# Optimization experiments

Measured on AMD Instinct MI355X. Metric: run time of the kernel, lower is better.

## Reference

```python
import jax, jax.numpy as jnp
import numpy as np

B, L, ENC_D, DEC_D, ATTN_D = 64, 1024, 512, 512, 512


def setup_inputs() -> dict:
    key = jax.random.key(0)
    ks = jax.random.split(key, 8)
    s_enc = 1.0 / np.sqrt(ENC_D)
    s_dec = 1.0 / np.sqrt(DEC_D)
    s_att = 1.0 / np.sqrt(ATTN_D)
    return {
        "enc_out": jax.random.normal(ks[0], (B, L, ENC_D), dtype=jnp.float32),
        "dec_hidden": jax.random.normal(ks[1], (B, DEC_D), dtype=jnp.float32),
        # nn.Linear params (uniform(-1/sqrt(fan_in), 1/sqrt(fan_in)))
        "W_enc": jax.random.uniform(ks[2], (ENC_D, ATTN_D), jnp.float32, -s_enc, s_enc),
        "b_enc": jax.random.uniform(ks[3], (ATTN_D,), jnp.float32, -s_enc, s_enc),
        "W_dec": jax.random.uniform(ks[4], (DEC_D, ATTN_D), jnp.float32, -s_dec, s_dec),
        "b_dec": jax.random.uniform(ks[5], (ATTN_D,), jnp.float32, -s_dec, s_dec),
        "W_full": jax.random.uniform(ks[6], (ATTN_D,), jnp.float32, -s_att, s_att),
        "b_full": jax.random.uniform(ks[7], (), jnp.float32, -s_att, s_att),
    }


def reference(enc_out, dec_hidden, W_enc, b_enc, W_dec, b_dec, W_full, b_full):
    # attn1: [B, L, A]; attn2: [B, A]
    attn1 = jnp.einsum("ble,ea->bla", enc_out, W_enc) + b_enc
    attn2 = dec_hidden @ W_dec + b_dec
    # full_attn(relu(attn1 + attn2[:, None])) -> [B, L]
    attn = jnp.einsum("bla,a->bl", jax.nn.relu(attn1 + attn2[:, None, :]), W_full) + b_full
    alpha = jax.nn.softmax(attn, axis=1)  # over L
    attn_weighted_enc = jnp.einsum("ble,bl->be", enc_out, alpha)
    return attn_weighted_enc, alpha
```

## Files before the change

### kernel.cpp

```cpp
#include <hip/hip_runtime.h>
#include <hip/hip_bf16.h>

typedef __bf16 bf16x8 __attribute__((ext_vector_type(8)));
typedef float f32x16 __attribute__((ext_vector_type(16)));
typedef unsigned int u32;
typedef unsigned short u16;

#define WS_WT     0
#define WS_BIAS   524288
#define WS_LOGITS 655360

__device__ __forceinline__ u16 f2bf(float f) {
    __bf16 h = (__bf16)f;
    return __builtin_bit_cast(u16, h);
}

__device__ __forceinline__ void gload_lds16(const void* g, void* l) {
    __builtin_amdgcn_global_load_lds(
        (const __attribute__((address_space(1))) u32*)g,
        (__attribute__((address_space(3))) u32*)l, 16, 0, 0);
}

__device__ __forceinline__ bf16x8 cvt8(float4 a, float4 b) {
    bf16x8 r;
    r[0] = (__bf16)a.x; r[1] = (__bf16)a.y; r[2] = (__bf16)a.z; r[3] = (__bf16)a.w;
    r[4] = (__bf16)b.x; r[5] = (__bf16)b.y; r[6] = (__bf16)b.z; r[7] = (__bf16)b.w;
    return r;
}

__global__ void k_wt(const float* __restrict__ W, u16* __restrict__ WtP) {
    int u = blockIdx.x * 256 + threadIdx.x;
    int l = u & 63, ks = (u >> 6) & 31, p = u >> 11;
    int n = p * 32 + (l & 31);
    int k0 = ks * 16 + (l >> 5) * 8;
    u16 o[8];
    #pragma unroll
    for (int e = 0; e < 8; ++e)
        o[e] = f2bf(W[(k0 + e) * 512 + n]);
    *(uint4*)(WtP + (size_t)u * 8) = *(const uint4*)o;
}

__global__ void k_bias2(const float* __restrict__ dec, const float* __restrict__ Wd,
                        const float* __restrict__ b_dec, const float* __restrict__ b_enc,
                        float* __restrict__ bias2p, float* __restrict__ out0) {
    int blk = blockIdx.x;
    int b = blk >> 2, nc = blk & 3;
    int t = threadIdx.x;
    if (blk < 64) {
        out0[blk * 512 + t * 2] = 0.f;
        out0[blk * 512 + t * 2 + 1] = 0.f;
    }
    __shared__ float sdec[512];
    __shared__ float red[256];
    for (int k = t; k < 512; k += 256) sdec[k] = dec[b * 512 + k];
    __syncthreads();
    int n = nc * 128 + (t & 127);
    int kh = t >> 7;
    float acc = 0.f;
    int k0 = kh * 256;
    #pragma unroll 4
    for (int k = k0; k < k0 + 256; ++k)
        acc += sdec[k] * Wd[k * 512 + n];
    red[t] = acc;
    __syncthreads();
    if (t < 128) {
        int nn = nc * 128 + t;
        bias2p[b * 512 + nn] = red[t] + red[t + 128] + b_dec[nn] + b_enc[nn];
    }
}

__global__ __launch_bounds__(256, 2) void k_logits(
        const float* __restrict__ enc, const u16* __restrict__ WtP,
        const float* __restrict__ bias2p, const float* __restrict__ Wf,
        float* __restrict__ logits) {
    __shared__ __align__(16) char ldsA[32768];
    __shared__ __align__(16) char ldsB0[16384];
    __shared__ __align__(16) char ldsB1[16384];

    int t = threadIdx.x;
    int lane = t & 63;
    int w = t >> 6;
    int blk = blockIdx.x;
    int b = blk >> 3;
    int cl = lane & 31;
    int hi = lane >> 5;

    #define STAGEB(buf, p_, h_)                                                   \
        {                                                                         \
            const char* s_ = (const char*)WtP + (size_t)(p_) * 32768              \
                             + (h_) * 16384 + t * 16;                             \
            _Pragma("unroll")                                                     \
            for (int j = 0; j < 4; ++j)                                           \
                gload_lds16(s_ + j * 4096, (char*)(buf) + t * 16 + j * 4096);     \
        }
    #define STAGEA(s_)                                                            \
        {                                                                         \
            size_t base_ = ((size_t)blk * 128 + (s_) * 16) * 2048;                \
            _Pragma("unroll")                                                     \
            for (int j = 0; j < 8; ++j) {                                         \
                int u_ = t + j * 256;                                             \
                int r_ = u_ >> 7, c_ = u_ & 127;                                  \
                const char* src_ = (const char*)enc + base_ + (size_t)r_ * 2048   \
                                   + ((size_t)(c_ ^ (r_ & 7)) * 16);              \
                gload_lds16(src_, ldsA + (size_t)u_ * 16);                        \
            }                                                                     \
        }

    STAGEB(ldsB0, 0, 0)
    STAGEA(0)

    bf16x8 A[32];
    int rloc = lane & 15;
    int myswz = rloc & 7;
    int parity = (lane >> 4) & 1;
    for (int s = 0; s < 8; ++s) {
        __syncthreads();
        if ((s >> 1) == w && (s & 1) == parity) {
            #pragma unroll
            for (int f = 0; f < 32; ++f) {
                int c0 = (f * 4 + hi * 2) ^ myswz;
                int c1 = (f * 4 + hi * 2 + 1) ^ myswz;
                float4 lo = *(const float4*)(ldsA + rloc * 2048 + c0 * 16);
                float4 h4 = *(const float4*)(ldsA + rloc * 2048 + c1 * 16);
                A[f] = cvt8(lo, h4);
            }
        }
        __syncthreads();
        if (s < 7) STAGEA(s + 1)
    }
    #pragma unroll
    for (int f = 0; f < 32; ++f)
        asm volatile("" : "+v"(A[f]));

    float pr[16];
    #pragma unroll
    for (int r = 0; r < 16; ++r) pr[r] = 0.f;

    for (int p = 0; p < 16; ++p) {
        __syncthreads();
        STAGEB(ldsB1, p, 1)
        f32x16 acc0 = {};
        #pragma unroll
        for (int i = 0; i < 16; ++i) {
            uint4 braw = *(const uint4*)(ldsB0 + i * 1024 + lane * 16);
            acc0 = __builtin_amdgcn_mfma_f32_32x32x16_bf16(
                A[i], __builtin_bit_cast(bf16x8, braw), acc0, 0, 0, 0);
        }
        __syncthreads();
        if (p < 15) STAGEB(ldsB0, p + 1, 0)
        f32x16 acc1 = {};
        #pragma unroll
        for (int i = 0; i < 16; ++i) {
            uint4 braw = *(const uint4*)(ldsB1 + i * 1024 + lane * 16);
            acc1 = __builtin_amdgcn_mfma_f32_32x32x16_bf16(
                A[16 + i], __builtin_bit_cast(bf16x8, braw), acc1, 0, 0, 0);
        }
        int col = p * 32 + cl;
        float bias = bias2p[b * 512 + col];
        float wfv = Wf[col];
        #pragma unroll
        for (int r = 0; r < 16; ++r) {
            float v = acc0[r] + acc1[r] + bias;
            v = v > 0.f ? v : 0.f;
            pr[r] += v * wfv;
        }
    }

    #pragma unroll
    for (int r = 0; r < 16; ++r) {
        float v = pr[r];
        v += __shfl_xor(v, 1, 64);
        v += __shfl_xor(v, 2, 64);
        v += __shfl_xor(v, 4, 64);
        v += __shfl_xor(v, 8, 64);
        v += __shfl_xor(v, 16, 64);
        if (cl == 0)
            logits[blk * 128 + w * 32 + (r & 3) + 8 * (r >> 2) + 4 * hi] = v;
    }
}

__global__ void k_softmax(const float* __restrict__ logits, float* __restrict__ alpha) {
    int b = blockIdx.x;
    int t = threadIdx.x;
    __shared__ float red[256];
    float4 v = ((const float4*)(logits + b * 1024))[t];
    float mx = fmaxf(fmaxf(v.x, v.y), fmaxf(v.z, v.w));
    red[t] = mx;
    __syncthreads();
    for (int s = 128; s > 0; s >>= 1) {
        if (t < s) red[t] = fmaxf(red[t], red[t + s]);
        __syncthreads();
    }
    mx = red[0];
    __syncthreads();
    float4 e;
    e.x = expf(v.x - mx); e.y = expf(v.y - mx);
    e.z = expf(v.z - mx); e.w = expf(v.w - mx);
    red[t] = e.x + e.y + e.z + e.w;
    __syncthreads();
    for (int s = 128; s > 0; s >>= 1) {
        if (t < s) red[t] += red[t + s];
        __syncthreads();
    }
    float inv = 1.0f / red[0];
    float4 o;
    o.x = e.x * inv; o.y = e.y * inv; o.z = e.z * inv; o.w = e.w * inv;
    ((float4*)(alpha + b * 1024))[t] = o;
}

__global__ void k_wsum_part(const float* __restrict__ enc, const float* __restrict__ alpha,
                            float* __restrict__ out) {
    int blk = blockIdx.x;
    int b = blk >> 3, c = blk & 7;
    int t = threadIdx.x;
    int col = (t & 127) * 4;
    int lh = t >> 7;
    const float* ep = enc + (size_t)(b * 1024 + c * 128) * 512;
    const float* al = alpha + b * 1024 + c * 128;
    float4 s = {0.f, 0.f, 0.f, 0.f};
    #pragma unroll 4
    for (int i = 0; i < 64; ++i) {
        int l = i * 2 + lh;
        float a = al[l];
        float4 e = *(const float4*)(ep + (size_t)l * 512 + col);
        s.x += e.x * a; s.y += e.y * a; s.z += e.z * a; s.w += e.w * a;
    }
    __shared__ float red[2][512];
    *(float4*)&red[lh][col] = s;
    __syncthreads();
    if (t < 128) {
        float4 a0 = *(const float4*)&red[0][t * 4];
        float4 a1 = *(const float4*)&red[1][t * 4];
        float* op = out + b * 512 + t * 4;
        atomicAdd(op + 0, a0.x + a1.x);
        atomicAdd(op + 1, a0.y + a1.y);
        atomicAdd(op + 2, a0.z + a1.z);
        atomicAdd(op + 3, a0.w + a1.w);
    }
}

extern "C" void kernel_launch(void* const* d_in, const int* in_sizes, int n_in,
                              void* d_out, int out_size, void* d_ws, size_t ws_size,
                              hipStream_t stream) {
    const float* enc    = (const float*)d_in[0];
    const float* dec    = (const float*)d_in[1];
    const float* W_enc  = (const float*)d_in[2];
    const float* b_enc  = (const float*)d_in[3];
    const float* W_dec  = (const float*)d_in[4];
    const float* b_dec  = (const float*)d_in[5];
    const float* W_full = (const float*)d_in[6];

    float* out = (float*)d_out;
    char* ws = (char*)d_ws;
    u16* WtP      = (u16*)(ws + WS_WT);
    float* bias2p = (float*)(ws + WS_BIAS);
    float* logits = (float*)(ws + WS_LOGITS);
    float* alpha  = out + 32768;

    hipLaunchKernelGGL(k_wt,        dim3(128), dim3(256), 0, stream, W_enc, WtP);
    hipLaunchKernelGGL(k_bias2,     dim3(256), dim3(256), 0, stream,
                       dec, W_dec, b_dec, b_enc, bias2p, out);
    hipLaunchKernelGGL(k_logits,    dim3(512), dim3(256), 0, stream,
                       enc, WtP, bias2p, W_full, logits);
    hipLaunchKernelGGL(k_softmax,   dim3(64),  dim3(256), 0, stream, logits, alpha);
    hipLaunchKernelGGL(k_wsum_part, dim3(512), dim3(256), 0, stream, enc, alpha, out);
}
```

Measured before the change: 106.6 us.

## Deepen LDS pipelining in logits kernel with double-buffered A and triple-buffered B

```diff
diff --git a/kernel.cpp b/kernel.cpp
--- a/kernel.cpp
+++ b/kernel.cpp
@@ -73,9 +73,7 @@
         const float* __restrict__ enc, const u16* __restrict__ WtP,
         const float* __restrict__ bias2p, const float* __restrict__ Wf,
         float* __restrict__ logits) {
-    __shared__ __align__(16) char ldsA[32768];
-    __shared__ __align__(16) char ldsB0[16384];
-    __shared__ __align__(16) char ldsB1[16384];
+    __shared__ __align__(16) char lds[69632];
 
     int t = threadIdx.x;
     int lane = t & 63;
@@ -84,16 +82,11 @@
     int b = blk >> 3;
     int cl = lane & 31;
     int hi = lane >> 5;
-
-    #define STAGEB(buf, p_, h_)                                                   \
-        {                                                                         \
-            const char* s_ = (const char*)WtP + (size_t)(p_) * 32768              \
-                             + (h_) * 16384 + t * 16;                             \
-            _Pragma("unroll")                                                     \
-            for (int j = 0; j < 4; ++j)                                           \
-                gload_lds16(s_ + j * 4096, (char*)(buf) + t * 16 + j * 4096);     \
-        }
-    #define STAGEA(s_)                                                            \
+    int rloc = lane & 15;
+    int parity = (lane >> 4) & 1;
+    int myswz = rloc & 7;
+
+    #define STAGEA(s_, X_)                                                        \
         {                                                                         \
             size_t base_ = ((size_t)blk * 128 + (s_) * 16) * 2048;                \
             _Pragma("unroll")                                                     \
@@ -102,68 +95,120 @@
                 int r_ = u_ >> 7, c_ = u_ & 127;                                  \
                 const char* src_ = (const char*)enc + base_ + (size_t)r_ * 2048   \
                                    + ((size_t)(c_ ^ (r_ & 7)) * 16);              \
-                gload_lds16(src_, ldsA + (size_t)u_ * 16);                        \
+                gload_lds16(src_, lds + (X_) + (size_t)u_ * 16);                  \
             }                                                                     \
         }
-
-    STAGEB(ldsB0, 0, 0)
-    STAGEA(0)
+    #define STAGEB(u_, off_)                                                      \
+        {                                                                         \
+            const char* s_ = (const char*)WtP + (size_t)(u_) * 16384 + t * 16;    \
+            _Pragma("unroll")                                                     \
+            for (int j = 0; j < 4; ++j)                                           \
+                gload_lds16(s_ + j * 4096, lds + (off_) + t * 16 + j * 4096);     \
+        }
+    #define REDIST(X_)                                                            \
+        {                                                                         \
+            _Pragma("unroll")                                                     \
+            for (int f = 0; f < 32; ++f) {                                        \
+                int c0 = (f * 4 + hi * 2) ^ myswz;                                \
+                int c1 = (f * 4 + hi * 2 + 1) ^ myswz;                            \
+                float4 lo = *(const float4*)(lds + (X_) + rloc * 2048 + c0 * 16); \
+                float4 h4 = *(const float4*)(lds + (X_) + rloc * 2048 + c1 * 16); \
+                A[f] = cvt8(lo, h4);                                              \
+            }                                                                     \
+        }
+
+    STAGEA(0, 0)
+    STAGEA(1, 32768)
+    if (w == 0) {
+        #pragma unroll
+        for (int j = 0; j < 2; ++j)
+            gload_lds16((const char*)(bias2p + b * 512 + j * 256) + lane * 16,
+                        lds + 65536 + j * 1024 + lane * 16);
+    } else if (w == 1) {
+        #pragma unroll
+        for (int j = 0; j < 2; ++j)
+            gload_lds16((const char*)(Wf + j * 256) + lane * 16,
+                        lds + 67584 + j * 1024 + lane * 16);
+    }
 
     bf16x8 A[32];
-    int rloc = lane & 15;
-    int myswz = rloc & 7;
-    int parity = (lane >> 4) & 1;
-    for (int s = 0; s < 8; ++s) {
-        __syncthreads();
-        if ((s >> 1) == w && (s & 1) == parity) {
-            #pragma unroll
-            for (int f = 0; f < 32; ++f) {
-                int c0 = (f * 4 + hi * 2) ^ myswz;
-                int c1 = (f * 4 + hi * 2 + 1) ^ myswz;
-                float4 lo = *(const float4*)(ldsA + rloc * 2048 + c0 * 16);
-                float4 h4 = *(const float4*)(ldsA + rloc * 2048 + c1 * 16);
-                A[f] = cvt8(lo, h4);
-            }
-        }
-        __syncthreads();
-        if (s < 7) STAGEA(s + 1)
-    }
+    for (int s = 0; s < 7; ++s) {
+        asm volatile("s_waitcnt vmcnt(8)" ::: "memory");
+        __builtin_amdgcn_s_barrier();
+        if ((s >> 1) == w && (s & 1) == parity) REDIST((s & 1) * 32768)
+        asm volatile("s_waitcnt lgkmcnt(0)" ::: "memory");
+        __builtin_amdgcn_s_barrier();
+        if (s < 6) STAGEA(s + 2, (s & 1) * 32768)
+    }
+    asm volatile("s_waitcnt vmcnt(0)" ::: "memory");
+    __builtin_amdgcn_s_barrier();
+    if (w == 3 && parity == 1) REDIST(32768)
+    asm volatile("s_waitcnt lgkmcnt(0)" ::: "memory");
+    __builtin_amdgcn_s_barrier();
     #pragma unroll
     for (int f = 0; f < 32; ++f)
         asm volatile("" : "+v"(A[f]));
 
+    STAGEB(0, 0)
+    STAGEB(1, 16384)
+    STAGEB(2, 32768)
+
     float pr[16];
     #pragma unroll
     for (int r = 0; r < 16; ++r) pr[r] = 0.f;
 
-    for (int p = 0; p < 16; ++p) {
-        __syncthreads();
-        STAGEB(ldsB1, p, 1)
+    #define CONSUME(accv, Abase, off_)                                            \
+        {                                                                         \
+            __builtin_amdgcn_s_setprio(1);                                        \
+            _Pragma("unroll")                                                     \
+            for (int i = 0; i < 16; ++i) {                                        \
+                uint4 braw = *(const uint4*)(lds + (off_) + i * 1024 + lane * 16);\
+                accv = __builtin_amdgcn_mfma_f32_32x32x16_bf16(                   \
+                    A[(Abase) + i], __builtin_bit_cast(bf16x8, braw), accv, 0, 0, 0); \
+            }                                                                     \
+            __builtin_amdgcn_s_setprio(0);                                        \
+        }
+    #define EPILOG(p_)                                                            \
+        {                                                                         \
+            float bias = *(const float*)(lds + 65536 + ((p_) * 32 + cl) * 4);     \
+            float wfv  = *(const float*)(lds + 67584 + ((p_) * 32 + cl) * 4);     \
+            _Pragma("unroll")                                                     \
+            for (int r = 0; r < 16; ++r) {                                        \
+                float v = acc0[r] + acc1[r] + bias;                               \
+                v = v > 0.f ? v : 0.f;                                            \
+                pr[r] += v * wfv;                                                 \
+            }                                                                     \
+        }
+
+    for (int p = 0; p < 15; ++p) {
+        int q = (p & 1) << 1;
+        int bufA = q * 16384;
+        int bufB = (q | 1) * 16384;
+        int stA = ((q ^ 2) | 1) * 16384;
+        int stB = (q ^ 2) * 16384;
+        stB = q * 16384;
+        asm volatile("s_waitcnt vmcnt(8)" ::: "memory");
+        __builtin_amdgcn_s_barrier();
+        STAGEB(2 * p + 3, stA)
         f32x16 acc0 = {};
-        #pragma unroll
-        for (int i = 0; i < 16; ++i) {
-            uint4 braw = *(const uint4*)(ldsB0 + i * 1024 + lane * 16);
-            acc0 = __builtin_amdgcn_mfma_f32_32x32x16_bf16(
-                A[i], __builtin_bit_cast(bf16x8, braw), acc0, 0, 0, 0);
-        }
-        __syncthreads();
-        if (p < 15) STAGEB(ldsB0, p + 1, 0)
+        CONSUME(acc0, 0, bufA)
+        asm volatile("s_waitcnt vmcnt(8)" ::: "memory");
+        __builtin_amdgcn_s_barrier();
+        if (p < 14) STAGEB(2 * p + 4, stB)
         f32x16 acc1 = {};
-        #pragma unroll
-        for (int i = 0; i < 16; ++i) {
-            uint4 braw = *(const uint4*)(ldsB1 + i * 1024 + lane * 16);
-            acc1 = __builtin_amdgcn_mfma_f32_32x32x16_bf16(
-                A[16 + i], __builtin_bit_cast(bf16x8, braw), acc1, 0, 0, 0);
-        }
-        int col = p * 32 + cl;
-        float bias = bias2p[b * 512 + col];
-        float wfv = Wf[col];
-        #pragma unroll
-        for (int r = 0; r < 16; ++r) {
-            float v = acc0[r] + acc1[r] + bias;
-            v = v > 0.f ? v : 0.f;
-            pr[r] += v * wfv;
-        }
+        CONSUME(acc1, 16, bufB)
+        EPILOG(p)
+    }
+    {
+        asm volatile("s_waitcnt vmcnt(4)" ::: "memory");
+        __builtin_amdgcn_s_barrier();
+        f32x16 acc0 = {};
+        CONSUME(acc0, 0, 32768)
+        asm volatile("s_waitcnt vmcnt(0)" ::: "memory");
+        __builtin_amdgcn_s_barrier();
+        f32x16 acc1 = {};
+        CONSUME(acc1, 16, 49152)
+        EPILOG(15)
     }
 
     #pragma unroll
```

New measurement: 112.8 us. 5.8% more time.

## Double-buffer A staging and B tiles in unified LDS with one barrier per step

Applied to the files above, without the earlier changes.

```diff
diff --git a/kernel.cpp b/kernel.cpp
--- a/kernel.cpp
+++ b/kernel.cpp
@@ -73,9 +73,7 @@
         const float* __restrict__ enc, const u16* __restrict__ WtP,
         const float* __restrict__ bias2p, const float* __restrict__ Wf,
         float* __restrict__ logits) {
-    __shared__ __align__(16) char ldsA[32768];
-    __shared__ __align__(16) char ldsB0[16384];
-    __shared__ __align__(16) char ldsB1[16384];
+    __shared__ __align__(16) char lds[65536];
 
     int t = threadIdx.x;
     int lane = t & 63;
@@ -84,16 +82,11 @@
     int b = blk >> 3;
     int cl = lane & 31;
     int hi = lane >> 5;
-
-    #define STAGEB(buf, p_, h_)                                                   \
-        {                                                                         \
-            const char* s_ = (const char*)WtP + (size_t)(p_) * 32768              \
-                             + (h_) * 16384 + t * 16;                             \
-            _Pragma("unroll")                                                     \
-            for (int j = 0; j < 4; ++j)                                           \
-                gload_lds16(s_ + j * 4096, (char*)(buf) + t * 16 + j * 4096);     \
-        }
-    #define STAGEA(s_)                                                            \
+    int rloc = lane & 15;
+    int parity = (lane >> 4) & 1;
+    int myswz = rloc & 7;
+
+    #define STAGEA(s_, X_)                                                        \
         {                                                                         \
             size_t base_ = ((size_t)blk * 128 + (s_) * 16) * 2048;                \
             _Pragma("unroll")                                                     \
@@ -102,58 +95,65 @@
                 int r_ = u_ >> 7, c_ = u_ & 127;                                  \
                 const char* src_ = (const char*)enc + base_ + (size_t)r_ * 2048   \
                                    + ((size_t)(c_ ^ (r_ & 7)) * 16);              \
-                gload_lds16(src_, ldsA + (size_t)u_ * 16);                        \
+                gload_lds16(src_, lds + (X_) + (size_t)u_ * 16);                  \
             }                                                                     \
         }
-
-    STAGEB(ldsB0, 0, 0)
-    STAGEA(0)
-
+    #define STAGEB(off_, p_, h_)                                                  \
+        {                                                                         \
+            const char* s_ = (const char*)WtP + (size_t)(p_) * 32768              \
+                             + (h_) * 16384 + t * 16;                             \
+            _Pragma("unroll")                                                     \
+            for (int j = 0; j < 4; ++j)                                           \
+                gload_lds16(s_ + j * 4096, lds + (off_) + t * 16 + j * 4096);     \
+        }
+    #define REDIST(X_)                                                            \
+        {                                                                         \
+            _Pragma("unroll")                                                     \
+            for (int f = 0; f < 32; ++f) {                                        \
+                int c0 = (f * 4 + hi * 2) ^ myswz;                                \
+                int c1 = (f * 4 + hi * 2 + 1) ^ myswz;                            \
+                float4 lo = *(const float4*)(lds + (X_) + rloc * 2048 + c0 * 16); \
+                float4 h4 = *(const float4*)(lds + (X_) + rloc * 2048 + c1 * 16); \
+                A[f] = cvt8(lo, h4);                                              \
+            }                                                                     \
+        }
+
+    STAGEA(0, 0)
     bf16x8 A[32];
-    int rloc = lane & 15;
-    int myswz = rloc & 7;
-    int parity = (lane >> 4) & 1;
     for (int s = 0; s < 8; ++s) {
         __syncthreads();
-        if ((s >> 1) == w && (s & 1) == parity) {
-            #pragma unroll
-            for (int f = 0; f < 32; ++f) {
-                int c0 = (f * 4 + hi * 2) ^ myswz;
-                int c1 = (f * 4 + hi * 2 + 1) ^ myswz;
-                float4 lo = *(const float4*)(ldsA + rloc * 2048 + c0 * 16);
-                float4 h4 = *(const float4*)(ldsA + rloc * 2048 + c1 * 16);
-                A[f] = cvt8(lo, h4);
-            }
-        }
-        __syncthreads();
-        if (s < 7) STAGEA(s + 1)
-    }
+        if (s < 7) STAGEA(s + 1, ((s + 1) & 1) * 32768)
+        if ((s >> 1) == w && (s & 1) == parity) REDIST((s & 1) * 32768)
+    }
+    __syncthreads();
     #pragma unroll
     for (int f = 0; f < 32; ++f)
         asm volatile("" : "+v"(A[f]));
 
+    STAGEB(0, 0, 0)
+    STAGEB(16384, 0, 1)
+
     float pr[16];
     #pragma unroll
     for (int r = 0; r < 16; ++r) pr[r] = 0.f;
 
     for (int p = 0; p < 16; ++p) {
         __syncthreads();
-        STAGEB(ldsB1, p, 1)
-        f32x16 acc0 = {};
+        int sl = (p & 1) * 32768;
+        int nsl = sl ^ 32768;
+        if (p < 15) {
+            STAGEB(nsl, p + 1, 0)
+            STAGEB(nsl + 16384, p + 1, 1)
+        }
+        f32x16 acc0 = {}, acc1 = {};
         #pragma unroll
         for (int i = 0; i < 16; ++i) {
-            uint4 braw = *(const uint4*)(ldsB0 + i * 1024 + lane * 16);
+            uint4 b0 = *(const uint4*)(lds + sl + i * 1024 + lane * 16);
+            uint4 b1 = *(const uint4*)(lds + sl + 16384 + i * 1024 + lane * 16);
             acc0 = __builtin_amdgcn_mfma_f32_32x32x16_bf16(
-                A[i], __builtin_bit_cast(bf16x8, braw), acc0, 0, 0, 0);
-        }
-        __syncthreads();
-        if (p < 15) STAGEB(ldsB0, p + 1, 0)
-        f32x16 acc1 = {};
-        #pragma unroll
-        for (int i = 0; i < 16; ++i) {
-            uint4 braw = *(const uint4*)(ldsB1 + i * 1024 + lane * 16);
+                A[i], __builtin_bit_cast(bf16x8, b0), acc0, 0, 0, 0);
             acc1 = __builtin_amdgcn_mfma_f32_32x32x16_bf16(
-                A[16 + i], __builtin_bit_cast(bf16x8, braw), acc1, 0, 0, 0);
+                A[16 + i], __builtin_bit_cast(bf16x8, b1), acc1, 0, 0, 0);
         }
         int col = p * 32 + cl;
         float bias = bias2p[b * 512 + col];
```

Result: no change. 106.7 us (+0.1%).
